# Kernel optimization log

Hardware: AMD Instinct MI355X
Metric: run time of the kernel (lower is better)

## Reference

```python
import jax, jax.numpy as jnp
import numpy as np

D = 64  # head_dim

def setup_inputs() -> dict:
    key = jax.random.key(0)
    ks = jax.random.split(key, 8)
    B, H, Lq, Lk = 2, 8, 512, 512
    s = 1.0 / np.sqrt(D)
    Q = jax.random.normal(ks[0], (B, H, Lq, D), dtype=jnp.float32)
    K = jax.random.normal(ks[1], (B, H, Lk, D), dtype=jnp.float32)
    W1 = jax.random.uniform(ks[2], (D, D), jnp.float32, -s, s)
    b1 = jax.random.uniform(ks[3], (D,), jnp.float32, -s, s)
    W2 = jax.random.uniform(ks[4], (D, D), jnp.float32, -s, s)
    b2 = jax.random.uniform(ks[5], (D,), jnp.float32, -s, s)
    V = jax.random.uniform(ks[6], (D, 1), jnp.float32, -s, s)
    bV = jax.random.uniform(ks[7], (1,), jnp.float32, -s, s)
    return {"Q": Q, "K": K, "W1": W1, "b1": b1, "W2": W2, "b2": b2, "V": V, "bV": bV}

def reference(Q, K, W1, b1, W2, b2, V, bV):
    # Project once per query/key (equivalent to Linear on broadcast tensors)
    Wq = jnp.einsum('bhqd,de->bhqe', Q, W1) + b1          # [B,H,Lq,D]
    Wk = jnp.einsum('bhkd,de->bhke', K, W2) + b2          # [B,H,Lk,D]
    feat = jnp.tanh(Wq[:, :, :, None, :] + Wk[:, :, None, :, :])  # [B,H,Lq,Lk,D]
    scores = jnp.einsum('bhqkd,d->bhqk', feat, V[:, 0]) + bV[0]   # [B,H,Lq,Lk]
    return scores
```

## Files before the change

kernel.cpp:

```cpp
#include <hip/hip_runtime.h>


#define BH 16
#define L 512
#define D 64
#define C_SCALE 2.8853900817779268f

__global__ __launch_bounds__(256) void proj_kernel(
    const float* __restrict__ Q, const float* __restrict__ K,
    const float* __restrict__ W1, const float* __restrict__ b1,
    const float* __restrict__ W2, const float* __restrict__ b2,
    float* __restrict__ eq_all, float* __restrict__ ek_all)
{
    int blk = blockIdx.x;
    bool isK = blk >= 2048;
    const float* __restrict__ X  = isK ? K  : Q;
    const float* __restrict__ W  = isK ? W2 : W1;
    const float* __restrict__ bb = isK ? b2 : b1;
    float* __restrict__ O = isK ? ek_all : eq_all;
    int rb = (isK ? blk - 2048 : blk) * 4;

    __shared__ float xs[4][64];
    int tid = threadIdx.x;
    xs[tid >> 6][tid & 63] = X[rb * 64 + tid];
    __syncthreads();

    int lr = tid >> 6;
    int e  = tid & 63;
    float a0 = 0.f, a1 = 0.f, a2 = 0.f, a3 = 0.f;
    #pragma unroll
    for (int d = 0; d < 64; d += 4) {
        a0 = fmaf(xs[lr][d + 0], W[(d + 0) * 64 + e], a0);
        a1 = fmaf(xs[lr][d + 1], W[(d + 1) * 64 + e], a1);
        a2 = fmaf(xs[lr][d + 2], W[(d + 2) * 64 + e], a2);
        a3 = fmaf(xs[lr][d + 3], W[(d + 3) * 64 + e], a3);
    }
    float r = ((a0 + a1) + (a2 + a3)) + bb[e];
    O[(rb + lr) * 64 + e] = __builtin_amdgcn_exp2f(r * C_SCALE);
}

#define PAIR(accref, q0, q1, k0, k1, v0, v1)          \
    {                                                  \
        float d0_  = fmaf((q0), (k0), 1.0f);           \
        float d1_  = fmaf((q1), (k1), 1.0f);           \
        float t_   = (v1) * d0_;                       \
        float num_ = fmaf((v0), d1_, t_);              \
        float pr_  = d0_ * d1_;                        \
        float rc_  = __builtin_amdgcn_rcpf(pr_);       \
        (accref)   = fmaf(num_, rc_, (accref));        \
    }

__global__ __launch_bounds__(256, 8) void score_kernel(
    const float* __restrict__ eq_all, const float* __restrict__ ek_all,
    const float* __restrict__ Vv, const float* __restrict__ bV,
    float* __restrict__ out)
{
    __shared__ float eq[32][68];
    __shared__ float ek[32][68];
    __shared__ float Vs[64];

    int tid = threadIdx.x;
    int blk = blockIdx.x;
    int kt = blk & 15;
    int qt = (blk >> 4) & 15;
    int bh = blk >> 8;

    const float4* __restrict__ eqg = (const float4*)(eq_all + (bh * L + qt * 32) * D);
    const float4* __restrict__ ekg = (const float4*)(ek_all + (bh * L + kt * 32) * D);

    #pragma unroll
    for (int i = 0; i < 2; ++i) {
        int idx = tid + i * 256;
        int r = idx >> 4, c4 = idx & 15;
        *(float4*)&eq[r][c4 * 4] = eqg[idx];
        *(float4*)&ek[r][c4 * 4] = ekg[idx];
    }
    if (tid < 64) Vs[tid] = Vv[tid];
    __syncthreads();

    int kg = tid & 15;
    int qg = tid >> 4;

    const float* __restrict__ eqp0 = &eq[qg][0];
    const float* __restrict__ eqp1 = &eq[qg + 16][0];
    const float* __restrict__ ekp0 = &ek[kg][0];
    const float* __restrict__ ekp1 = &ek[kg + 16][0];

    float acc00 = 0.f, acc01 = 0.f, acc10 = 0.f, acc11 = 0.f;

    #pragma unroll 8
    for (int d4 = 0; d4 < 16; ++d4) {
        float4 vq0 = *(const float4*)(eqp0 + d4 * 4);
        float4 vq1 = *(const float4*)(eqp1 + d4 * 4);
        float4 vk0 = *(const float4*)(ekp0 + d4 * 4);
        float4 vk1 = *(const float4*)(ekp1 + d4 * 4);
        float4 vv  = *(const float4*)&Vs[d4 * 4];

        PAIR(acc00, vq0.x, vq0.y, vk0.x, vk0.y, vv.x, vv.y);
        PAIR(acc00, vq0.z, vq0.w, vk0.z, vk0.w, vv.z, vv.w);
        PAIR(acc01, vq0.x, vq0.y, vk1.x, vk1.y, vv.x, vv.y);
        PAIR(acc01, vq0.z, vq0.w, vk1.z, vk1.w, vv.z, vv.w);
        PAIR(acc10, vq1.x, vq1.y, vk0.x, vk0.y, vv.x, vv.y);
        PAIR(acc10, vq1.z, vq1.w, vk0.z, vk0.w, vv.z, vv.w);
        PAIR(acc11, vq1.x, vq1.y, vk1.x, vk1.y, vv.x, vv.y);
        PAIR(acc11, vq1.z, vq1.w, vk1.z, vk1.w, vv.z, vv.w);
    }

    float sv = 0.f;
    #pragma unroll
    for (int d4 = 0; d4 < 16; ++d4) {
        float4 vv = *(const float4*)&Vs[d4 * 4];
        sv += (vv.x + vv.y) + (vv.z + vv.w);
    }

    float base = bV[0] + sv;
    int o00 = (bh * L + qt * 32 + qg) * L + kt * 32 + kg;
    out[o00]              = fmaf(-2.f, acc00, base);
    out[o00 + 16]         = fmaf(-2.f, acc01, base);
    out[o00 + 16 * L]     = fmaf(-2.f, acc10, base);
    out[o00 + 16 * L + 16] = fmaf(-2.f, acc11, base);
}

extern "C" void kernel_launch(void* const* d_in, const int* in_sizes, int n_in,
                              void* d_out, int out_size, void* d_ws, size_t ws_size,
                              hipStream_t stream) {
    const float* Q  = (const float*)d_in[0];
    const float* K  = (const float*)d_in[1];
    const float* W1 = (const float*)d_in[2];
    const float* b1 = (const float*)d_in[3];
    const float* W2 = (const float*)d_in[4];
    const float* b2 = (const float*)d_in[5];
    const float* V  = (const float*)d_in[6];
    const float* bV = (const float*)d_in[7];
    float* out = (float*)d_out;

    float* eq_all = (float*)d_ws;
    float* ek_all = eq_all + BH * L * D;

    proj_kernel<<<4096, 256, 0, stream>>>(Q, K, W1, b1, W2, b2, eq_all, ek_all);
    score_kernel<<<4096, 256, 0, stream>>>(eq_all, ek_all, V, bV, out);
}
```

Measured before the change: 113.6 us.

## Merge four tanh terms per reciprocal and enlarge score tiles to 64x64

The score kernel now combines four head-dimension terms into one fraction, so each reciprocal covers four tanh contributions instead of two. The tile per block grows from 32x32 to 64x64, with each thread computing a 4x4 output block from shared-memory rows, which improves operand reuse. The grid shrinks to 1024 blocks and the occupancy hint drops to 4 blocks per SM. The change raises register pressure and the risk of overflow in the four-way product of denominators.

New measurement: 110.7 us. 1.03x faster.

```diff
diff --git a/kernel.cpp b/kernel.cpp
--- a/kernel.cpp
+++ b/kernel.cpp
@@ -39,41 +39,45 @@
     O[(rb + lr) * 64 + e] = __builtin_amdgcn_exp2f(r * C_SCALE);
 }
 
-#define PAIR(accref, q0, q1, k0, k1, v0, v1)          \
-    {                                                  \
-        float d0_  = fmaf((q0), (k0), 1.0f);           \
-        float d1_  = fmaf((q1), (k1), 1.0f);           \
-        float t_   = (v1) * d0_;                       \
-        float num_ = fmaf((v0), d1_, t_);              \
-        float pr_  = d0_ * d1_;                        \
-        float rc_  = __builtin_amdgcn_rcpf(pr_);       \
-        (accref)   = fmaf(num_, rc_, (accref));        \
+#define QUAD(accref, q_, k_, v_)                                   \
+    {                                                               \
+        float d0_ = fmaf((q_).x, (k_).x, 1.0f);                     \
+        float d1_ = fmaf((q_).y, (k_).y, 1.0f);                     \
+        float d2_ = fmaf((q_).z, (k_).z, 1.0f);                     \
+        float d3_ = fmaf((q_).w, (k_).w, 1.0f);                     \
+        float d01_ = d0_ * d1_;                                     \
+        float d23_ = d2_ * d3_;                                     \
+        float n01_ = fmaf((v_).x, d1_, (v_).y * d0_);               \
+        float n23_ = fmaf((v_).z, d3_, (v_).w * d2_);               \
+        float num_ = fmaf(n23_, d01_, n01_ * d23_);                 \
+        float rc_  = __builtin_amdgcn_rcpf(d01_ * d23_);            \
+        (accref)   = fmaf(num_, rc_, (accref));                     \
     }
 
-__global__ __launch_bounds__(256, 8) void score_kernel(
+__global__ __launch_bounds__(256, 4) void score_kernel(
     const float* __restrict__ eq_all, const float* __restrict__ ek_all,
     const float* __restrict__ Vv, const float* __restrict__ bV,
     float* __restrict__ out)
 {
-    __shared__ float eq[32][68];
-    __shared__ float ek[32][68];
+    __shared__ float eq[64][68];
+    __shared__ float ek[64][68];
     __shared__ float Vs[64];
 
     int tid = threadIdx.x;
     int blk = blockIdx.x;
-    int kt = blk & 15;
-    int qt = (blk >> 4) & 15;
-    int bh = blk >> 8;
+    int kt = blk & 7;
+    int qt = (blk >> 3) & 7;
+    int bh = blk >> 6;
 
-    const float4* __restrict__ eqg = (const float4*)(eq_all + (bh * L + qt * 32) * D);
-    const float4* __restrict__ ekg = (const float4*)(ek_all + (bh * L + kt * 32) * D);
+    const float4* __restrict__ eqg = (const float4*)(eq_all + (bh * L + qt * 64) * D);
+    const float4* __restrict__ ekg = (const float4*)(ek_all + (bh * L + kt * 64) * D);
 
     #pragma unroll
-    for (int i = 0; i < 2; ++i) {
+    for (int i = 0; i < 8; ++i) {
         int idx = tid + i * 256;
         int r = idx >> 4, c4 = idx & 15;
-        *(float4*)&eq[r][c4 * 4] = eqg[idx];
-        *(float4*)&ek[r][c4 * 4] = ekg[idx];
+        if (r < 64) *(float4*)&eq[r][c4 * 4] = eqg[idx];
+        else        *(float4*)&ek[r - 64][c4 * 4] = ekg[idx - 1024];
     }
     if (tid < 64) Vs[tid] = Vv[tid];
     __syncthreads();
@@ -81,44 +85,47 @@
     int kg = tid & 15;
     int qg = tid >> 4;
 
-    const float* __restrict__ eqp0 = &eq[qg][0];
-    const float* __restrict__ eqp1 = &eq[qg + 16][0];
-    const float* __restrict__ ekp0 = &ek[kg][0];
-    const float* __restrict__ ekp1 = &ek[kg + 16][0];
+    float acc[4][4] = {{0.f,0.f,0.f,0.f},{0.f,0.f,0.f,0.f},
+                       {0.f,0.f,0.f,0.f},{0.f,0.f,0.f,0.f}};
 
-    float acc00 = 0.f, acc01 = 0.f, acc10 = 0.f, acc11 = 0.f;
-
-    #pragma unroll 8
+    #pragma unroll 4
     for (int d4 = 0; d4 < 16; ++d4) {
-        float4 vq0 = *(const float4*)(eqp0 + d4 * 4);
-        float4 vq1 = *(const float4*)(eqp1 + d4 * 4);
-        float4 vk0 = *(const float4*)(ekp0 + d4 * 4);
-        float4 vk1 = *(const float4*)(ekp1 + d4 * 4);
+        float4 vq0 = *(const float4*)&eq[qg     ][d4 * 4];
+        float4 vq1 = *(const float4*)&eq[qg + 16][d4 * 4];
+        float4 vq2 = *(const float4*)&eq[qg + 32][d4 * 4];
+        float4 vq3 = *(const float4*)&eq[qg + 48][d4 * 4];
+        float4 vk0 = *(const float4*)&ek[kg     ][d4 * 4];
+        float4 vk1 = *(const float4*)&ek[kg + 16][d4 * 4];
+        float4 vk2 = *(const float4*)&ek[kg + 32][d4 * 4];
+        float4 vk3 = *(const float4*)&ek[kg + 48][d4 * 4];
         float4 vv  = *(const float4*)&Vs[d4 * 4];
 
-        PAIR(acc00, vq0.x, vq0.y, vk0.x, vk0.y, vv.x, vv.y);
-        PAIR(acc00, vq0.z, vq0.w, vk0.z, vk0.w, vv.z, vv.w);
-        PAIR(acc01, vq0.x, vq0.y, vk1.x, vk1.y, vv.x, vv.y);
-        PAIR(acc01, vq0.z, vq0.w, vk1.z, vk1.w, vv.z, vv.w);
-        PAIR(acc10, vq1.x, vq1.y, vk0.x, vk0.y, vv.x, vv.y);
-        PAIR(acc10, vq1.z, vq1.w, vk0.z, vk0.w, vv.z, vv.w);
-        PAIR(acc11, vq1.x, vq1.y, vk1.x, vk1.y, vv.x, vv.y);
-        PAIR(acc11, vq1.z, vq1.w, vk1.z, vk1.w, vv.z, vv.w);
+        QUAD(acc[0][0], vq0, vk0, vv); QUAD(acc[0][1], vq0, vk1, vv);
+        QUAD(acc[0][2], vq0, vk2, vv); QUAD(acc[0][3], vq0, vk3, vv);
+        QUAD(acc[1][0], vq1, vk0, vv); QUAD(acc[1][1], vq1, vk1, vv);
+        QUAD(acc[1][2], vq1, vk2, vv); QUAD(acc[1][3], vq1, vk3, vv);
+        QUAD(acc[2][0], vq2, vk0, vv); QUAD(acc[2][1], vq2, vk1, vv);
+        QUAD(acc[2][2], vq2, vk2, vv); QUAD(acc[2][3], vq2, vk3, vv);
+        QUAD(acc[3][0], vq3, vk0, vv); QUAD(acc[3][1], vq3, vk1, vv);
+        QUAD(acc[3][2], vq3, vk2, vv); QUAD(acc[3][3], vq3, vk3, vv);
     }
 
     float sv = 0.f;
     #pragma unroll
-    for (int d4 = 0; d4 < 16; ++d4) {
-        float4 vv = *(const float4*)&Vs[d4 * 4];
+    for (int t = 0; t < 16; ++t) {
+        float4 vv = *(const float4*)&Vs[t * 4];
         sv += (vv.x + vv.y) + (vv.z + vv.w);
     }
 
     float base = bV[0] + sv;
-    int o00 = (bh * L + qt * 32 + qg) * L + kt * 32 + kg;
-    out[o00]              = fmaf(-2.f, acc00, base);
-    out[o00 + 16]         = fmaf(-2.f, acc01, base);
-    out[o00 + 16 * L]     = fmaf(-2.f, acc10, base);
-    out[o00 + 16 * L + 16] = fmaf(-2.f, acc11, base);
+    int orow = (bh * L + qt * 64 + qg) * L + kt * 64 + kg;
+    #pragma unroll
+    for (int i = 0; i < 4; ++i) {
+        #pragma unroll
+        for (int j = 0; j < 4; ++j) {
+            out[orow + (16 * i) * L + 16 * j] = fmaf(-2.f, acc[i][j], base);
+        }
+    }
 }
 
 extern "C" void kernel_launch(void* const* d_in, const int* in_sizes, int n_in,
@@ -138,5 +145,5 @@
     float* ek_all = eq_all + BH * L * D;
 
     proj_kernel<<<4096, 256, 0, stream>>>(Q, K, W1, b1, W2, b2, eq_all, ek_all);
-    score_kernel<<<4096, 256, 0, stream>>>(eq_all, ek_all, V, bV, out);
+    score_kernel<<<1024, 256, 0, stream>>>(eq_all, ek_all, V, bV, out);
 }
```
